# Performance work log

Hardware: AMD Instinct MI355X
Metric: run time of the kernel (lower is better)

## Reference

```python
import jax, jax.numpy as jnp
import numpy as np

TEMP = 20.0
ATT_WT = 0.5
EPS = 1e-12


def _l2n(x, axis):
    return x / jnp.maximum(jnp.linalg.norm(x, axis=axis, keepdims=True), EPS)


def _conv2d(x, w, b, pad, dil):
    y = jax.lax.conv_general_dilated(
        x, w, window_strides=(1, 1), padding=[(pad, pad), (pad, pad)],
        rhs_dilation=(dil, dil), dimension_numbers=("NCHW", "OIHW", "NCHW"))
    return y + b[None, :, None, None]


def _maxpool3(x):
    return jax.lax.reduce_window(x, -jnp.inf, jax.lax.max,
                                 (1, 1, 3, 3), (1, 1, 3, 3), "VALID")


def setup_inputs() -> dict:
    key = jax.random.key(0)
    ks = jax.random.split(key, 8)
    L, B, C, h, w = 9, 4, 512, 32, 32
    sc = 0.05
    return {
        "fq_feats": jax.random.normal(ks[0], (L, B, C, h, w), jnp.float32),
        "fs_feats": jax.random.normal(ks[1], (L, B, C, h, w), jnp.float32),
        "f_q": jax.random.normal(ks[2], (B, C, h, w), jnp.float32),
        "f_s": jax.random.normal(ks[3], (B, C, h, w), jnp.float32),
        "w1": jax.random.normal(ks[4], (256, 1024, 3, 3), jnp.float32) * sc,
        "b1": jnp.zeros((256,), jnp.float32),
        "w2": jax.random.normal(ks[5], (256, 256, 3, 3), jnp.float32) * sc,
        "b2": jnp.zeros((256,), jnp.float32),
        "w3": jax.random.normal(ks[6], (1, 256, 3, 3), jnp.float32) * sc,
        "b3": jnp.zeros((1,), jnp.float32),
    }


def reference(fq_feats, fs_feats, f_q, f_s, w1, b1, w2, b2, w3, b3):
    B, C, h, w = f_q.shape
    # per-level cosine correlation volumes: normalize over channel dim
    fq_n = _l2n(fq_feats, axis=2)  # [L,B,C,h,w]
    fs_n = _l2n(fs_feats, axis=2)
    corr = jnp.einsum("lbcxy,lbcuv->lbxyuv", fq_n, fs_n)  # [L,B,h,w,h,w]
    # MatchNet corr_forward: ReLU'd volumes fused across hyperpixel levels,
    # temperature softmax over support positions, aggregate support values v=f_s
    corr = jax.nn.relu(corr).mean(axis=0)                 # [B,h,w,h,w]
    attn = jax.nn.softmax(corr.reshape(B, h * w, h * w) * TEMP, axis=-1)
    att_fq = jnp.einsum("bqs,bcs->bcq", attn, f_s.reshape(B, C, h * w))
    att_fq = att_fq.reshape(B, C, h, w)
    fq = _l2n(f_q, axis=1) + _l2n(att_fq, axis=1) * ATT_WT
    # AttentionBranch (Dropout2d is identity at inference)
    comp = jnp.concatenate((f_q, f_s), axis=1)            # [B,1024,h,w]
    x = jax.nn.relu(_conv2d(comp, w1, b1, pad=2, dil=2))  # [B,256,32,32]
    x = _conv2d(x, w2, b2, pad=0, dil=1)                  # [B,256,30,30]
    x = _maxpool3(x)                                      # [B,256,10,10]
    x = _conv2d(x, w3, b3, pad=0, dil=1)                  # [B,1,8,8]
    weight = x.mean(axis=(2, 3)).squeeze()[None]          # [1,B]
    return fq, att_fq, weight
```

## Files before the change

### kernel.cpp

```cpp
#include <hip/hip_runtime.h>
#include <hip/hip_bf16.h>

#define DI __device__ __forceinline__

typedef short bf16x8_t __attribute__((ext_vector_type(8)));
typedef _Float16 f16x8_t __attribute__((ext_vector_type(8)));
typedef float f32x4_t __attribute__((ext_vector_type(4)));

DI unsigned short f2bf(float f) {
    unsigned u = __float_as_uint(f);
    u += 0x7fffu + ((u >> 16) & 1u);
    return (unsigned short)(u >> 16);
}
DI float bfu2f(unsigned short u) { return __uint_as_float(((unsigned)u) << 16); }
DI unsigned short f2h(float f) {
    _Float16 h = (_Float16)f;
    unsigned short u;
    __builtin_memcpy(&u, &h, 2);
    return u;
}
DI float h2f(unsigned short u) {
    _Float16 h;
    __builtin_memcpy(&h, &u, 2);
    return (float)h;
}

__global__ __launch_bounds__(256) void k_prep(const float* __restrict__ fqf,
                                              const float* __restrict__ fsf,
                                              unsigned short* __restrict__ fqb,
                                              unsigned short* __restrict__ fsb) {
    __shared__ float T[128 * 33];
    __shared__ float red[512];
    __shared__ float invn[128];
    const int pt = blockIdx.x;
    const int lb = blockIdx.y;
    const int tz = blockIdx.z;
    const float* src = (tz ? fsf : fqf) + (size_t)lb * 524288 + pt * 128;
    unsigned short* dst = (tz ? fsb : fqb) + (((size_t)(lb * 8 + pt)) << 16);
    const int t = threadIdx.x;

    {
        const int p2 = (t & 63) * 2, cg = t >> 6;
        const float* ap = src + (((size_t)(cg * 128)) << 10) + p2;
        float s0 = 0.f, s1 = 0.f;
        for (int c = 0; c < 128; ++c) {
            float2 v = *(const float2*)(ap + ((size_t)c << 10));
            s0 += v.x * v.x;
            s1 += v.y * v.y;
        }
        red[t] = s0;
        red[256 + t] = s1;
        __syncthreads();
        if (t < 64) {
            float a0 = red[t] + red[t + 64] + red[t + 128] + red[t + 192];
            float a1 = red[256 + t] + red[320 + t] + red[384 + t] + red[448 + t];
            invn[2 * t]     = 1.f / fmaxf(sqrtf(a0), 1e-12f);
            invn[2 * t + 1] = 1.f / fmaxf(sqrtf(a1), 1e-12f);
        }
    }

    for (int ks = 0; ks < 16; ++ks) {
        __syncthreads();
#pragma unroll
        for (int j = 0; j < 4; ++j) {
            int f = t + (j << 8);
            int row = f >> 5;
            int m4 = (f & 31) << 2;
            float4 v = *(const float4*)(src + (((size_t)(ks * 32 + row)) << 10) + m4);
            T[(m4 + 0) * 33 + row] = v.x;
            T[(m4 + 1) * 33 + row] = v.y;
            T[(m4 + 2) * 33 + row] = v.z;
            T[(m4 + 3) * 33 + row] = v.w;
        }
        __syncthreads();
#pragma unroll
        for (int i = 0; i < 2; ++i) {
            int c = t + (i << 8);
            int m = c >> 2;
            int q = (c & 3) ^ ((m >> 2) & 3);
            const float* Tp = &T[m * 33 + q * 8];
            float iv = invn[m];
            uint4 r4;
            r4.x = (unsigned)f2h(Tp[0] * iv) | ((unsigned)f2h(Tp[1] * iv) << 16);
            r4.y = (unsigned)f2h(Tp[2] * iv) | ((unsigned)f2h(Tp[3] * iv) << 16);
            r4.z = (unsigned)f2h(Tp[4] * iv) | ((unsigned)f2h(Tp[5] * iv) << 16);
            r4.w = (unsigned)f2h(Tp[6] * iv) | ((unsigned)f2h(Tp[7] * iv) << 16);
            *(uint4*)(dst + ((size_t)ks << 12) + ((size_t)c << 3)) = r4;
        }
    }
}

__global__ __launch_bounds__(256) void k_corr2(const unsigned short* __restrict__ fqb,
                                               const unsigned short* __restrict__ fsb,
                                               unsigned short* __restrict__ P01) {
    __shared__ __align__(16) char L[2][16384];
    const int id = blockIdx.x;
    const int z = id & 7, local = id >> 3;
    const int b = z >> 1, lg = z & 1;
    const int qt = local >> 3, st = local & 7;
    const int q0 = qt * 128, s0 = st * 128;
    const int t = threadIdx.x;
    const int w = t >> 6, lane = t & 63;
    const int wrow = w >> 1, wcol = w & 1;
    const int quad = lane >> 4, m16 = lane & 15;
    const int nsteps = (5 - lg) << 4;

    f32x4_t zero4 = {0.f, 0.f, 0.f, 0.f};
    f32x4_t master[4][4], lvl[4][4];
#pragma unroll
    for (int i = 0; i < 4; ++i)
#pragma unroll
        for (int j = 0; j < 4; ++j) { master[i][j] = zero4; lvl[i][j] = zero4; }

    auto stage = [&](int step, int buf) {
        int g = step >> 4, ks = step & 15;
        int lb = (lg + 2 * g) * 4 + b;
        const unsigned short* Ab = fqb + ((((size_t)lb * 8 + qt) * 16 + ks) << 12);
        const unsigned short* Bb = fsb + ((((size_t)lb * 8 + st) * 16 + ks) << 12);
#pragma unroll
        for (int i = 0; i < 4; ++i) {
            int idx0 = i * 256 + w * 64;
            int idx = idx0 + lane;
            const unsigned short* srcp = (idx0 < 512)
                ? (Ab + ((size_t)idx << 3))
                : (Bb + ((size_t)(idx - 512) << 3));
            __builtin_amdgcn_global_load_lds(
                (const __attribute__((address_space(1))) void*)srcp,
                (__attribute__((address_space(3))) void*)(&L[buf][0] + idx0 * 16),
                16, 0, 0);
        }
    };

    stage(0, 0);
    for (int step = 0; step < nsteps; ++step) {
        const int buf = step & 1;
        __syncthreads();
        if (step < nsteps - 1) stage(step + 1, buf ^ 1);
        const char* base = &L[buf][0];
        f16x8_t af[4], bfr[4];
#pragma unroll
        for (int i = 0; i < 4; ++i) {
            int m = wrow * 64 + i * 16 + m16;
            int sa = quad ^ ((m >> 2) & 3);
            af[i] = *(const f16x8_t*)(base + m * 64 + sa * 16);
            int n = wcol * 64 + i * 16 + m16;
            int sb = quad ^ ((n >> 2) & 3);
            bfr[i] = *(const f16x8_t*)(base + 8192 + n * 64 + sb * 16);
        }
#pragma unroll
        for (int mi = 0; mi < 4; ++mi)
#pragma unroll
            for (int ni = 0; ni < 4; ++ni)
                lvl[mi][ni] = __builtin_amdgcn_mfma_f32_16x16x32_f16(
                    af[mi], bfr[ni], lvl[mi][ni], 0, 0, 0);

        if ((step & 15) == 15) {
#pragma unroll
            for (int mi = 0; mi < 4; ++mi)
#pragma unroll
                for (int ni = 0; ni < 4; ++ni) {
#pragma unroll
                    for (int e = 0; e < 4; ++e)
                        master[mi][ni][e] += fmaxf(lvl[mi][ni][e], 0.f);
                    lvl[mi][ni] = zero4;
                }
        }
    }

#pragma unroll
    for (int mi = 0; mi < 4; ++mi)
#pragma unroll
        for (int e = 0; e < 4; ++e) {
            int q = q0 + wrow * 64 + mi * 16 + quad * 4 + e;
            unsigned short* cp = P01 + ((((size_t)(lg * 4 + b)) * 1024 + q) << 10)
                                 + s0 + wcol * 64 + m16;
#pragma unroll
            for (int ni = 0; ni < 4; ++ni)
                cp[ni * 16] = f2h(master[mi][ni][e]);
        }
}

__global__ __launch_bounds__(256) void k_softmax(const unsigned short* __restrict__ P01,
                                                 unsigned short* __restrict__ attn) {
    __shared__ float red[8];
    const int row = blockIdx.x;
    const int b = row >> 10, q = row & 1023;
    const int t = threadIdx.x;
    const unsigned short* p0 = P01 + (((size_t)b << 20) + ((size_t)q << 10)) + t * 4;
    const unsigned short* p1 = p0 + ((size_t)4 << 20);
    uint2 a0 = *(const uint2*)p0;
    uint2 a1 = *(const uint2*)p1;
    const float SC = 20.f / 9.f;
    float v0 = (h2f(a0.x & 0xffff) + h2f(a1.x & 0xffff)) * SC;
    float v1 = (h2f(a0.x >> 16)    + h2f(a1.x >> 16)) * SC;
    float v2 = (h2f(a0.y & 0xffff) + h2f(a1.y & 0xffff)) * SC;
    float v3 = (h2f(a0.y >> 16)    + h2f(a1.y >> 16)) * SC;
    float m = fmaxf(fmaxf(v0, v1), fmaxf(v2, v3));
#pragma unroll
    for (int off = 32; off >= 1; off >>= 1) m = fmaxf(m, __shfl_down(m, off));
    const int wid = t >> 6, lane = t & 63;
    if (lane == 0) red[wid] = m;
    __syncthreads();
    m = fmaxf(fmaxf(red[0], red[1]), fmaxf(red[2], red[3]));
    float e0 = __expf(v0 - m), e1 = __expf(v1 - m);
    float e2 = __expf(v2 - m), e3 = __expf(v3 - m);
    float s = e0 + e1 + e2 + e3;
#pragma unroll
    for (int off = 32; off >= 1; off >>= 1) s += __shfl_down(s, off);
    if (lane == 0) red[4 + wid] = s;
    __syncthreads();
    s = red[4] + red[5] + red[6] + red[7];
    float inv = 1.f / s;
    unsigned short* o = attn + (size_t)((b * 32 + (t >> 3)) * 1024 + q) * 36 + (t & 7) * 4;
    uint2 r;
    r.x = (unsigned)f2h(e0 * inv) | ((unsigned)f2h(e1 * inv) << 16);
    r.y = (unsigned)f2h(e2 * inv) | ((unsigned)f2h(e3 * inv) << 16);
    *(uint2*)o = r;
}

__global__ __launch_bounds__(256) void k_fspack(const float* __restrict__ fsi,
                                                unsigned short* __restrict__ fsp) {
    int id = blockIdx.x * 256 + threadIdx.x;
    int c = id & 511, sb = (id >> 9) & 31, b = id >> 14;
    const float4* src = (const float4*)(fsi + (((size_t)(b * 512 + c)) << 10) + sb * 32);
    unsigned short* dst = fsp + (size_t)((b * 32 + sb) * 512 + c) * 36;
#pragma unroll
    for (int j = 0; j < 8; ++j) {
        float4 v = src[j];
        uint2 r;
        r.x = (unsigned)f2h(v.x) | ((unsigned)f2h(v.y) << 16);
        r.y = (unsigned)f2h(v.z) | ((unsigned)f2h(v.w) << 16);
        *(uint2*)(dst + j * 4) = r;
    }
}

__global__ __launch_bounds__(256) void k_attfqm(const unsigned short* __restrict__ fsp,
                                                const unsigned short* __restrict__ attn,
                                                float* __restrict__ attfq) {
    __shared__ __align__(16) char L[2][14336];
    const int q0 = blockIdx.x * 128;
    const int c0 = blockIdx.y * 64;
    const int b  = blockIdx.z;
    const int t = threadIdx.x;
    const int w = t >> 6, lane = t & 63;
    const int quad = lane >> 4, m16 = lane & 15;

    f32x4_t acc[4][2];
#pragma unroll
    for (int i = 0; i < 4; ++i)
#pragma unroll
        for (int j = 0; j < 2; ++j) acc[i][j] = (f32x4_t){0.f, 0.f, 0.f, 0.f};

    auto stage = [&](int sb, int buf) {
        const char* sa = (const char*)(fsp + (size_t)((b * 32 + sb) * 512 + c0) * 36);
        const char* sbp = (const char*)(attn + (size_t)((b * 32 + sb) * 1024 + q0) * 36);
#pragma unroll
        for (int i = 0; i < 4; ++i) {
            int idx0 = i * 256 + w * 64;
            if (idx0 < 896) {
                int idx = idx0 + lane;
                const char* src = (idx < 288) ? (sa + idx * 16) : (sbp + (idx - 288) * 16);
                __builtin_amdgcn_global_load_lds(
                    (const __attribute__((address_space(1))) void*)src,
                    (__attribute__((address_space(3))) void*)(&L[buf][0] + idx0 * 16),
                    16, 0, 0);
            }
        }
    };

    stage(0, 0);
    for (int sb = 0; sb < 32; ++sb) {
        const int buf = sb & 1;
        __syncthreads();
        if (sb < 31) stage(sb + 1, buf ^ 1);
        const char* base = &L[buf][0];
        f16x8_t af[4], bfr[2];
#pragma unroll
        for (int i = 0; i < 4; ++i) {
            const char* ap = base + (size_t)(i * 16 + m16) * 72 + quad * 16;
            union { unsigned long long d[2]; f16x8_t v; } u;
            u.d[0] = *(const unsigned long long*)ap;
            u.d[1] = *(const unsigned long long*)(ap + 8);
            af[i] = u.v;
        }
#pragma unroll
        for (int ni = 0; ni < 2; ++ni) {
            const char* bp = base + 4608 + (size_t)(w * 32 + ni * 16 + m16) * 72 + quad * 16;
            union { unsigned long long d[2]; f16x8_t v; } u;
            u.d[0] = *(const unsigned long long*)bp;
            u.d[1] = *(const unsigned long long*)(bp + 8);
            bfr[ni] = u.v;
        }
#pragma unroll
        for (int mi = 0; mi < 4; ++mi)
#pragma unroll
            for (int ni = 0; ni < 2; ++ni)
                acc[mi][ni] = __builtin_amdgcn_mfma_f32_16x16x32_f16(
                    af[mi], bfr[ni], acc[mi][ni], 0, 0, 0);
    }

#pragma unroll
    for (int mi = 0; mi < 4; ++mi)
#pragma unroll
        for (int e = 0; e < 4; ++e) {
            int c = c0 + mi * 16 + quad * 4 + e;
            float* rowp = attfq + (((size_t)(b * 512 + c)) << 10) + q0 + w * 32 + m16;
#pragma unroll
            for (int ni = 0; ni < 2; ++ni)
                rowp[ni * 16] = acc[mi][ni][e];
        }
}

__global__ __launch_bounds__(256) void k_out(const float* __restrict__ fqi,
                                             const float* __restrict__ attfq,
                                             float* __restrict__ out) {
    __shared__ float redq[256], reda[256];
    __shared__ float rnq[64], rna[64];
    const int b = blockIdx.y;
    const int p0 = blockIdx.x * 64;
    const int t = threadIdx.x;
    const int pl = t & 63, cg = t >> 6;
    const int pos = p0 + pl;
    const float* qp = fqi + (((size_t)b) << 19) + pos;
    const float* ap = attfq + (((size_t)b) << 19) + pos;
    float sq = 0.f, sa = 0.f;
    for (int c = cg * 128; c < cg * 128 + 128; ++c) {
        float q = qp[(size_t)c << 10];
        float a = ap[(size_t)c << 10];
        sq += q * q;
        sa += a * a;
    }
    redq[t] = sq; reda[t] = sa;
    __syncthreads();
    if (t < 64) {
        float q = redq[t] + redq[t + 64] + redq[t + 128] + redq[t + 192];
        float a = reda[t] + reda[t + 64] + reda[t + 128] + reda[t + 192];
        rnq[t] = 1.f / fmaxf(sqrtf(q), 1e-12f);
        rna[t] = 1.f / fmaxf(sqrtf(a), 1e-12f);
    }
    __syncthreads();
    const float RQ = rnq[pl], RA = 0.5f * rna[pl];
    float* o1 = out + (((size_t)b) << 19) + pos;
    float* o2 = o1 + 2097152;
    for (int c = cg * 128; c < cg * 128 + 128; ++c) {
        float q = qp[(size_t)c << 10];
        float a = ap[(size_t)c << 10];
        o1[(size_t)c << 10] = q * RQ + a * RA;
        o2[(size_t)c << 10] = a;
    }
}

__global__ __launch_bounds__(256) void k_w1pack(const float* __restrict__ w1,
                                                unsigned short* __restrict__ w1p) {
    int pid = blockIdx.x * 256 + threadIdx.x;
    int oc = pid >> 10, ic = pid & 1023;
    const float* src = w1 + (size_t)pid * 9;
    float f[9];
#pragma unroll
    for (int tp = 0; tp < 9; ++tp) f[tp] = src[tp];
    int s = ic >> 5, j = ic & 31;
#pragma unroll
    for (int tp = 0; tp < 9; ++tp) {
        size_t row = ((size_t)(tp * 32 + s) * 256 + oc) * 40;
        w1p[row + j] = f2bf(f[tp]);
        if (j < 8) w1p[row + 32 + j] = 0;
    }
}

__global__ __launch_bounds__(256) void k_conv1m(const float* __restrict__ fqi,
                                                const float* __restrict__ fsi,
                                                const unsigned short* __restrict__ w1p,
                                                float* __restrict__ P) {
    __shared__ __align__(16) char As[2][20480];
    __shared__ __align__(16) char Bs[2][4096];
    const int p0 = blockIdx.x * 64;
    const int b = blockIdx.y;
    const int tap = blockIdx.z;
    const int dy = 2 * (tap / 3) - 2;
    const int dx = 2 * (tap % 3) - 2;
    const int t = threadIdx.x;
    const int w = t >> 6, lane = t & 63;
    const int quad = lane >> 4, m16 = lane & 15;
    const int bn = t & 63, kg = t >> 6;
    const int e0 = p0 + bn;
    const bool valid = ((unsigned)((e0 >> 5) + dy) < 32u) &&
                       ((unsigned)((e0 & 31) + dx) < 32u);
    const int cidx = min(max(e0 + dy * 32 + dx, 0), 1023);
    const int bchunk = (bn * 4 + (kg ^ (bn & 3))) * 16;

    f32x4_t acc[4][4];
#pragma unroll
    for (int i = 0; i < 4; ++i)
#pragma unroll
        for (int j = 0; j < 4; ++j) acc[i][j] = (f32x4_t){0.f, 0.f, 0.f, 0.f};

    auto stageA = [&](int s, int buf) {
        const char* src = (const char*)(w1p + (size_t)(tap * 32 + s) * 10240);
#pragma unroll
        for (int i = 0; i < 5; ++i) {
            int idx = i * 4 + w;
            __builtin_amdgcn_global_load_lds(
                (const __attribute__((address_space(1))) void*)(src + idx * 1024 + lane * 16),
                (__attribute__((address_space(3))) void*)(&As[buf][0] + idx * 1024),
                16, 0, 0);
        }
    };
    auto stageB = [&](int s, int buf) {
        int ch = s * 32 + kg * 8;
        const float* plane = (ch < 512)
            ? (fqi + (((size_t)(b * 512 + ch)) << 10))
            : (fsi + (((size_t)(b * 512 + ch - 512)) << 10));
        float f[8];
#pragma unroll
        for (int j = 0; j < 8; ++j) {
            float v = plane[((size_t)j << 10) + cidx];
            f[j] = valid ? v : 0.f;
        }
        uint4 r4;
        r4.x = (unsigned)f2bf(f[0]) | ((unsigned)f2bf(f[1]) << 16);
        r4.y = (unsigned)f2bf(f[2]) | ((unsigned)f2bf(f[3]) << 16);
        r4.z = (unsigned)f2bf(f[4]) | ((unsigned)f2bf(f[5]) << 16);
        r4.w = (unsigned)f2bf(f[6]) | ((unsigned)f2bf(f[7]) << 16);
        *(uint4*)(&Bs[buf][bchunk]) = r4;
    };

    stageA(0, 0);
    stageB(0, 0);

    for (int s = 0; s < 32; ++s) {
        const int buf = s & 1;
        __syncthreads();
        if (s < 31) {
            stageA(s + 1, buf ^ 1);
            stageB(s + 1, buf ^ 1);
        }
        bf16x8_t af[4], bfr[4];
#pragma unroll
        for (int i = 0; i < 4; ++i) {
            af[i] = *(const bf16x8_t*)(&As[buf][0] + (size_t)(w * 64 + i * 16 + m16) * 80 + quad * 16);
            int nn = i * 16 + m16;
            bfr[i] = *(const bf16x8_t*)(&Bs[buf][0] + (nn * 4 + (quad ^ (nn & 3))) * 16);
        }
#pragma unroll
        for (int mi = 0; mi < 4; ++mi)
#pragma unroll
            for (int ni = 0; ni < 4; ++ni)
                acc[mi][ni] = __builtin_amdgcn_mfma_f32_16x16x32_bf16(
                    af[mi], bfr[ni], acc[mi][ni], 0, 0, 0);
    }

    float* Pb = P + (((size_t)(tap * 4 + b)) << 18) + p0;
#pragma unroll
    for (int mi = 0; mi < 4; ++mi)
#pragma unroll
        for (int e = 0; e < 4; ++e) {
            int oc = w * 64 + mi * 16 + quad * 4 + e;
            float* row = Pb + (size_t)oc * 1024 + m16;
#pragma unroll
            for (int ni = 0; ni < 4; ++ni)
                row[ni * 16] = acc[mi][ni][e];
        }
}

__global__ __launch_bounds__(256) void k_c1comb(const float* __restrict__ P,
                                                const float* __restrict__ b1,
                                                unsigned short* __restrict__ x1) {
    int id = blockIdx.x * 256 + threadIdx.x;
    int oc = (id >> 8) & 255;
    const float4* P4 = (const float4*)P;
    float bb = b1[oc];
    float4 a = P4[id];
    a.x += bb; a.y += bb; a.z += bb; a.w += bb;
#pragma unroll
    for (int tp = 1; tp < 9; ++tp) {
        float4 v = P4[id + tp * 262144];
        a.x += v.x; a.y += v.y; a.z += v.z; a.w += v.w;
    }
    float o0 = fmaxf(a.x, 0.f);
    float o1 = fmaxf(a.y, 0.f);
    float o2 = fmaxf(a.z, 0.f);
    float o3 = fmaxf(a.w, 0.f);
    uint2 r;
    r.x = (unsigned)f2bf(o0) | ((unsigned)f2bf(o1) << 16);
    r.y = (unsigned)f2bf(o2) | ((unsigned)f2bf(o3) << 16);
    ((uint2*)x1)[id] = r;
}

__global__ __launch_bounds__(256) void k_w2pack(const float* __restrict__ w2,
                                                unsigned short* __restrict__ w2p) {
    int pid = blockIdx.x * 256 + threadIdx.x;
    int oc = pid >> 8, ic = pid & 255;
    const float* src = w2 + (size_t)pid * 9;
    float f[9];
#pragma unroll
    for (int tp = 0; tp < 9; ++tp) f[tp] = src[tp];
    int s = ic >> 5, j = ic & 31;
#pragma unroll
    for (int tp = 0; tp < 9; ++tp) {
        size_t row = ((size_t)(tp * 8 + s) * 256 + oc) * 40;
        w2p[row + j] = f2bf(f[tp]);
        if (j < 8) w2p[row + 32 + j] = 0;
    }
}

__global__ __launch_bounds__(256) void k_conv2m(const unsigned short* __restrict__ x1,
                                                const unsigned short* __restrict__ w2p,
                                                float* __restrict__ P2) {
    __shared__ __align__(16) char As[2][20480];
    __shared__ __align__(16) char Bs[2][4096];
    const int p0 = blockIdx.x * 64;
    const int b = blockIdx.y;
    const int tap = blockIdx.z;
    const int t = threadIdx.x;
    const int w = t >> 6, lane = t & 63;
    const int quad = lane >> 4, m16 = lane & 15;
    const int bn = t & 63, kg = t >> 6;
    const int e0 = p0 + bn;
    const int cidx = min(e0 + (tap / 3) * 32 + (tap % 3), 1023);
    const int bchunk = (bn * 4 + (kg ^ (bn & 3))) * 16;

    f32x4_t acc[4][4];
#pragma unroll
    for (int i = 0; i < 4; ++i)
#pragma unroll
        for (int j = 0; j < 4; ++j) acc[i][j] = (f32x4_t){0.f, 0.f, 0.f, 0.f};

    auto stageA = [&](int s, int buf) {
        const char* src = (const char*)(w2p + (size_t)(tap * 8 + s) * 10240);
#pragma unroll
        for (int i = 0; i < 5; ++i) {
            int idx = i * 4 + w;
            __builtin_amdgcn_global_load_lds(
                (const __attribute__((address_space(1))) void*)(src + idx * 1024 + lane * 16),
                (__attribute__((address_space(3))) void*)(&As[buf][0] + idx * 1024),
                16, 0, 0);
        }
    };
    auto stageB = [&](int s, int buf) {
        int ch = s * 32 + kg * 8;
        const unsigned short* plane = x1 + (((size_t)(b * 256 + ch)) << 10);
        unsigned short u[8];
#pragma unroll
        for (int j = 0; j < 8; ++j) u[j] = plane[((size_t)j << 10) + cidx];
        uint4 r4;
        r4.x = (unsigned)u[0] | ((unsigned)u[1] << 16);
        r4.y = (unsigned)u[2] | ((unsigned)u[3] << 16);
        r4.z = (unsigned)u[4] | ((unsigned)u[5] << 16);
        r4.w = (unsigned)u[6] | ((unsigned)u[7] << 16);
        *(uint4*)(&Bs[buf][bchunk]) = r4;
    };

    stageA(0, 0);
    stageB(0, 0);

    for (int s = 0; s < 8; ++s) {
        const int buf = s & 1;
        __syncthreads();
        if (s < 7) {
            stageA(s + 1, buf ^ 1);
            stageB(s + 1, buf ^ 1);
        }
        bf16x8_t af[4], bfr[4];
#pragma unroll
        for (int i = 0; i < 4; ++i) {
            af[i] = *(const bf16x8_t*)(&As[buf][0] + (size_t)(w * 64 + i * 16 + m16) * 80 + quad * 16);
            int nn = i * 16 + m16;
            bfr[i] = *(const bf16x8_t*)(&Bs[buf][0] + (nn * 4 + (quad ^ (nn & 3))) * 16);
        }
#pragma unroll
        for (int mi = 0; mi < 4; ++mi)
#pragma unroll
            for (int ni = 0; ni < 4; ++ni)
                acc[mi][ni] = __builtin_amdgcn_mfma_f32_16x16x32_bf16(
                    af[mi], bfr[ni], acc[mi][ni], 0, 0, 0);
    }

    float* Pb = P2 + (((size_t)(tap * 4 + b)) << 18) + p0;
#pragma unroll
    for (int mi = 0; mi < 4; ++mi)
#pragma unroll
        for (int e = 0; e < 4; ++e) {
            int oc = w * 64 + mi * 16 + quad * 4 + e;
            float* row = Pb + (size_t)oc * 1024 + m16;
#pragma unroll
            for (int ni = 0; ni < 4; ++ni)
                row[ni * 16] = acc[mi][ni][e];
        }
}

__global__ __launch_bounds__(256) void k_c2pool(const float* __restrict__ P2,
                                                const float* __restrict__ b2,
                                                float* __restrict__ xp) {
    int id = blockIdx.x * 256 + threadIdx.x;
    int px = id % 10;
    int tmp = id / 10;
    int py = tmp % 10;
    int ch = tmp / 10;
    int b = ch >> 8, oc = ch & 255;
    float bb = b2[oc];
    float m = -3.4e38f;
#pragma unroll
    for (int dy = 0; dy < 3; ++dy)
#pragma unroll
        for (int dx = 0; dx < 3; ++dx) {
            int pos = (3 * py + dy) * 32 + 3 * px + dx;
            float v = bb;
#pragma unroll
            for (int tp = 0; tp < 9; ++tp)
                v += P2[(((size_t)(tp * 4 + b)) << 18) + (size_t)oc * 1024 + pos];
            m = fmaxf(m, v);
        }
    xp[id] = m;
}

__global__ __launch_bounds__(256) void k_conv3(const float* __restrict__ xp,
                                               const float* __restrict__ w3,
                                               const float* __restrict__ b3,
                                               float* __restrict__ out) {
    __shared__ float s[256];
    int b = blockIdx.x, t = threadIdx.x;
    int pos = t & 63, qi = t >> 6;
    int y = pos >> 3, x = pos & 7;
    float acc = 0.f;
    for (int ic = qi * 64; ic < qi * 64 + 64; ++ic) {
        const float* ip = xp + ((size_t)(b * 256 + ic)) * 100 + y * 10 + x;
#pragma unroll
        for (int kh = 0; kh < 3; ++kh)
#pragma unroll
            for (int kw = 0; kw < 3; ++kw)
                acc = fmaf(w3[ic * 9 + kh * 3 + kw], ip[kh * 10 + kw], acc);
    }
    s[t] = acc;
    __syncthreads();
    if (t < 64) {
        float v = s[t] + s[t + 64] + s[t + 128] + s[t + 192];
#pragma unroll
        for (int off = 32; off >= 1; off >>= 1) v += __shfl_down(v, off);
        if (t == 0) out[4194304 + b] = v * (1.f / 64.f) + b3[0];
    }
}

extern "C" void kernel_launch(void* const* d_in, const int* in_sizes, int n_in,
                              void* d_out, int out_size, void* d_ws, size_t ws_size,
                              hipStream_t stream) {
    (void)in_sizes; (void)n_in; (void)out_size; (void)ws_size;
    const float* fqf = (const float*)d_in[0];
    const float* fsf = (const float*)d_in[1];
    const float* fqi = (const float*)d_in[2];
    const float* fsi = (const float*)d_in[3];
    const float* w1  = (const float*)d_in[4];
    const float* b1  = (const float*)d_in[5];
    const float* w2  = (const float*)d_in[6];
    const float* b2  = (const float*)d_in[7];
    const float* w3  = (const float*)d_in[8];
    const float* b3  = (const float*)d_in[9];
    float* out = (float*)d_out;

    float* W = (float*)d_ws;
    unsigned short* P01u = (unsigned short*)W;
    float* attfq = W;
    unsigned short* attn = (unsigned short*)(W + 4194304);
    unsigned short* w1p  = (unsigned short*)(W + 4194304);
    unsigned short* w2p  = (unsigned short*)(W + 4194304);
    unsigned short* fsp = (unsigned short*)(W + 6553600);
    unsigned short* x1 = (unsigned short*)(W + 7733248);
    float* xp = W + 8257536;
    unsigned short* fqb = (unsigned short*)(W + 8359936);
    float* P9 = W + 8359936;
    unsigned short* fsb = (unsigned short*)(W + 17797120);

    hipLaunchKernelGGL(k_w1pack,  dim3(1024),      dim3(256), 0, stream, w1, w1p);
    hipLaunchKernelGGL(k_conv1m,  dim3(16, 4, 9),  dim3(256), 0, stream, fqi, fsi, w1p, P9);
    hipLaunchKernelGGL(k_c1comb,  dim3(1024),      dim3(256), 0, stream, P9, b1, x1);
    hipLaunchKernelGGL(k_fspack,  dim3(256),       dim3(256), 0, stream, fsi, fsp);
    hipLaunchKernelGGL(k_prep,    dim3(8, 36, 2),  dim3(256), 0, stream, fqf, fsf, fqb, fsb);
    hipLaunchKernelGGL(k_corr2,   dim3(512),       dim3(256), 0, stream, fqb, fsb, P01u);
    hipLaunchKernelGGL(k_softmax, dim3(4096),      dim3(256), 0, stream, P01u, attn);
    hipLaunchKernelGGL(k_attfqm,  dim3(8, 8, 4),   dim3(256), 0, stream, fsp, attn, attfq);
    hipLaunchKernelGGL(k_out,     dim3(16, 4),     dim3(256), 0, stream, fqi, attfq, out);
    hipLaunchKernelGGL(k_w2pack,  dim3(256),       dim3(256), 0, stream, w2, w2p);
    hipLaunchKernelGGL(k_conv2m,  dim3(16, 4, 9),  dim3(256), 0, stream, x1, w2p, P9);
    hipLaunchKernelGGL(k_c2pool,  dim3(400),       dim3(256), 0, stream, P9, b2, xp);
    hipLaunchKernelGGL(k_conv3,   dim3(4),         dim3(256), 0, stream, xp, w3, b3, out);
}
```

Baseline: 501.1 us.

## Fold L2 normalization into corr epilogue and read prep input once

```diff
diff --git a/kernel.cpp b/kernel.cpp
--- a/kernel.cpp
+++ b/kernel.cpp
@@ -28,70 +28,89 @@
 __global__ __launch_bounds__(256) void k_prep(const float* __restrict__ fqf,
                                               const float* __restrict__ fsf,
                                               unsigned short* __restrict__ fqb,
-                                              unsigned short* __restrict__ fsb) {
+                                              unsigned short* __restrict__ fsb,
+                                              float* __restrict__ rq,
+                                              float* __restrict__ rs) {
     __shared__ float T[128 * 33];
-    __shared__ float red[512];
-    __shared__ float invn[128];
     const int pt = blockIdx.x;
     const int lb = blockIdx.y;
     const int tz = blockIdx.z;
     const float* src = (tz ? fsf : fqf) + (size_t)lb * 524288 + pt * 128;
     unsigned short* dst = (tz ? fsb : fqb) + (((size_t)(lb * 8 + pt)) << 16);
+    float* rdst = (tz ? rs : rq) + lb * 1024 + pt * 128;
     const int t = threadIdx.x;
 
-    {
-        const int p2 = (t & 63) * 2, cg = t >> 6;
-        const float* ap = src + (((size_t)(cg * 128)) << 10) + p2;
-        float s0 = 0.f, s1 = 0.f;
-        for (int c = 0; c < 128; ++c) {
-            float2 v = *(const float2*)(ap + ((size_t)c << 10));
-            s0 += v.x * v.x;
-            s1 += v.y * v.y;
-        }
-        red[t] = s0;
-        red[256 + t] = s1;
-        __syncthreads();
-        if (t < 64) {
-            float a0 = red[t] + red[t + 64] + red[t + 128] + red[t + 192];
-            float a1 = red[256 + t] + red[320 + t] + red[384 + t] + red[448 + t];
-            invn[2 * t]     = 1.f / fmaxf(sqrtf(a0), 1e-12f);
-            invn[2 * t + 1] = 1.f / fmaxf(sqrtf(a1), 1e-12f);
-        }
-    }
-
-    for (int ks = 0; ks < 16; ++ks) {
-        __syncthreads();
+    const int m0 = t >> 2, m1 = 64 + (t >> 2);
+    const int q0 = (t & 3) ^ ((m0 >> 2) & 3);
+    const int q1 = (t & 3) ^ ((m1 >> 2) & 3);
+    float ssq0 = 0.f, ssq1 = 0.f;
+
+    const int brow = t >> 5;
+    float4 v[4];
+    auto load = [&](int ks) {
 #pragma unroll
         for (int j = 0; j < 4; ++j) {
             int f = t + (j << 8);
             int row = f >> 5;
             int m4 = (f & 31) << 2;
-            float4 v = *(const float4*)(src + (((size_t)(ks * 32 + row)) << 10) + m4);
-            T[(m4 + 0) * 33 + row] = v.x;
-            T[(m4 + 1) * 33 + row] = v.y;
-            T[(m4 + 2) * 33 + row] = v.z;
-            T[(m4 + 3) * 33 + row] = v.w;
-        }
+            v[j] = *(const float4*)(src + (((size_t)(ks * 32 + row)) << 10) + m4);
+        }
+    };
+
+    load(0);
+    for (int ks = 0; ks < 16; ++ks) {
         __syncthreads();
 #pragma unroll
-        for (int i = 0; i < 2; ++i) {
-            int c = t + (i << 8);
-            int m = c >> 2;
-            int q = (c & 3) ^ ((m >> 2) & 3);
-            const float* Tp = &T[m * 33 + q * 8];
-            float iv = invn[m];
+        for (int j = 0; j < 4; ++j) {
+            int f = t + (j << 8);
+            int row = f >> 5;
+            int m4 = (f & 31) << 2;
+            T[(m4 + 0) * 33 + row] = v[j].x;
+            T[(m4 + 1) * 33 + row] = v[j].y;
+            T[(m4 + 2) * 33 + row] = v[j].z;
+            T[(m4 + 3) * 33 + row] = v[j].w;
+        }
+        __syncthreads();
+        if (ks < 15) load(ks + 1);
+        {
+            const float* Tp = &T[m0 * 33 + q0 * 8];
+            float f0 = Tp[0], f1 = Tp[1], f2 = Tp[2], f3 = Tp[3];
+            float f4 = Tp[4], f5 = Tp[5], f6 = Tp[6], f7 = Tp[7];
+            ssq0 += f0 * f0 + f1 * f1 + f2 * f2 + f3 * f3 +
+                    f4 * f4 + f5 * f5 + f6 * f6 + f7 * f7;
             uint4 r4;
-            r4.x = (unsigned)f2h(Tp[0] * iv) | ((unsigned)f2h(Tp[1] * iv) << 16);
-            r4.y = (unsigned)f2h(Tp[2] * iv) | ((unsigned)f2h(Tp[3] * iv) << 16);
-            r4.z = (unsigned)f2h(Tp[4] * iv) | ((unsigned)f2h(Tp[5] * iv) << 16);
-            r4.w = (unsigned)f2h(Tp[6] * iv) | ((unsigned)f2h(Tp[7] * iv) << 16);
-            *(uint4*)(dst + ((size_t)ks << 12) + ((size_t)c << 3)) = r4;
-        }
+            r4.x = (unsigned)f2h(f0) | ((unsigned)f2h(f1) << 16);
+            r4.y = (unsigned)f2h(f2) | ((unsigned)f2h(f3) << 16);
+            r4.z = (unsigned)f2h(f4) | ((unsigned)f2h(f5) << 16);
+            r4.w = (unsigned)f2h(f6) | ((unsigned)f2h(f7) << 16);
+            *(uint4*)(dst + ((size_t)ks << 12) + ((size_t)t << 3)) = r4;
+        }
+        {
+            const float* Tp = &T[m1 * 33 + q1 * 8];
+            float f0 = Tp[0], f1 = Tp[1], f2 = Tp[2], f3 = Tp[3];
+            float f4 = Tp[4], f5 = Tp[5], f6 = Tp[6], f7 = Tp[7];
+            ssq1 += f0 * f0 + f1 * f1 + f2 * f2 + f3 * f3 +
+                    f4 * f4 + f5 * f5 + f6 * f6 + f7 * f7;
+            uint4 r4;
+            r4.x = (unsigned)f2h(f0) | ((unsigned)f2h(f1) << 16);
+            r4.y = (unsigned)f2h(f2) | ((unsigned)f2h(f3) << 16);
+            r4.z = (unsigned)f2h(f4) | ((unsigned)f2h(f5) << 16);
+            r4.w = (unsigned)f2h(f6) | ((unsigned)f2h(f7) << 16);
+            *(uint4*)(dst + ((size_t)ks << 12) + ((size_t)(t + 256) << 3)) = r4;
+        }
+    }
+    ssq0 += __shfl_xor(ssq0, 1); ssq0 += __shfl_xor(ssq0, 2);
+    ssq1 += __shfl_xor(ssq1, 1); ssq1 += __shfl_xor(ssq1, 2);
+    if ((t & 3) == 0) {
+        rdst[m0] = 1.f / fmaxf(sqrtf(ssq0), 1e-12f);
+        rdst[m1] = 1.f / fmaxf(sqrtf(ssq1), 1e-12f);
     }
 }
 
 __global__ __launch_bounds__(256) void k_corr2(const unsigned short* __restrict__ fqb,
                                                const unsigned short* __restrict__ fsb,
+                                               const float* __restrict__ rq,
+                                               const float* __restrict__ rs,
                                                unsigned short* __restrict__ P01) {
     __shared__ __align__(16) char L[2][16384];
     const int id = blockIdx.x;
@@ -155,13 +174,24 @@
                     af[mi], bfr[ni], lvl[mi][ni], 0, 0, 0);
 
         if ((step & 15) == 15) {
+            int lb = (lg + 2 * (step >> 4)) * 4 + b;
+            const float* rqb = rq + lb * 1024 + q0 + wrow * 64;
+            const float* rsb = rs + lb * 1024 + s0 + wcol * 64;
+            float rq4[4][4], rsv[4];
+#pragma unroll
+            for (int mi = 0; mi < 4; ++mi) {
+                float4 vv = *(const float4*)(rqb + mi * 16 + quad * 4);
+                rq4[mi][0] = vv.x; rq4[mi][1] = vv.y; rq4[mi][2] = vv.z; rq4[mi][3] = vv.w;
+            }
+#pragma unroll
+            for (int ni = 0; ni < 4; ++ni) rsv[ni] = rsb[ni * 16 + m16];
 #pragma unroll
             for (int mi = 0; mi < 4; ++mi)
 #pragma unroll
                 for (int ni = 0; ni < 4; ++ni) {
 #pragma unroll
                     for (int e = 0; e < 4; ++e)
-                        master[mi][ni][e] += fmaxf(lvl[mi][ni][e], 0.f);
+                        master[mi][ni][e] += fmaxf(lvl[mi][ni][e] * rq4[mi][e] * rsv[ni], 0.f);
                     lvl[mi][ni] = zero4;
                 }
         }
@@ -661,6 +691,8 @@
     float* attfq = W;
     unsigned short* attn = (unsigned short*)(W + 4194304);
     unsigned short* w1p  = (unsigned short*)(W + 4194304);
+    float* rq = W + 5668864;
+    float* rs = W + 5705728;
     unsigned short* w2p  = (unsigned short*)(W + 4194304);
     unsigned short* fsp = (unsigned short*)(W + 6553600);
     unsigned short* x1 = (unsigned short*)(W + 7733248);
@@ -673,8 +705,8 @@
     hipLaunchKernelGGL(k_conv1m,  dim3(16, 4, 9),  dim3(256), 0, stream, fqi, fsi, w1p, P9);
     hipLaunchKernelGGL(k_c1comb,  dim3(1024),      dim3(256), 0, stream, P9, b1, x1);
     hipLaunchKernelGGL(k_fspack,  dim3(256),       dim3(256), 0, stream, fsi, fsp);
-    hipLaunchKernelGGL(k_prep,    dim3(8, 36, 2),  dim3(256), 0, stream, fqf, fsf, fqb, fsb);
-    hipLaunchKernelGGL(k_corr2,   dim3(512),       dim3(256), 0, stream, fqb, fsb, P01u);
+    hipLaunchKernelGGL(k_prep,    dim3(8, 36, 2),  dim3(256), 0, stream, fqf, fsf, fqb, fsb, rq, rs);
+    hipLaunchKernelGGL(k_corr2,   dim3(512),       dim3(256), 0, stream, fqb, fsb, rq, rs, P01u);
     hipLaunchKernelGGL(k_softmax, dim3(4096),      dim3(256), 0, stream, P01u, attn);
     hipLaunchKernelGGL(k_attfqm,  dim3(8, 8, 4),   dim3(256), 0, stream, fsp, attn, attfq);
     hipLaunchKernelGGL(k_out,     dim3(16, 4),     dim3(256), 0, stream, fqi, attfq, out);
```

New measurement: 450.9 us. 10.0% less time.
